# Kernel optimization log

Hardware: AMD Instinct MI355X
Metric: run time of the kernel (lower is better)

Reference implementation:

```python
import jax, jax.numpy as jnp
import numpy as np

B, P, N = 32, 64, 8192
EPS_CASE = 0.0001  # hard-coded threshold in fc_of_edge's tf.where


def setup_inputs() -> dict:
    key = jax.random.key(0)
    k1, k2 = jax.random.split(key)
    points = jax.random.normal(k1, (B, P, 2), dtype=jnp.float32)
    # phi grid comes from fc_tensor[0, 0, :] in the original ctor; use angles in [0, 2*pi)
    phi = jax.random.uniform(k2, (N,), dtype=jnp.float32) * (2.0 * np.pi)
    return {"points": points, "phi": phi}


def reference(points, phi):
    # q(phi) = [cos(phi), sin(phi) - 1], shape [2, N]
    q = jnp.stack([jnp.cos(phi), jnp.sin(phi) - 1.0])
    cross = jnp.array([[0.0, -1.0], [1.0, 0.0]], dtype=points.dtype)
    q_cross = cross @ q                                   # [2, N]
    scale = 1.0 / jnp.abs(q[0] ** 2 + q[1] ** 2)          # [N], real

    # vectorize the python edge loop: edge k is (points[:, k-1], points[:, k])
    p1 = points                                           # [B, P, 2]
    p0 = jnp.roll(points, 1, axis=1)                      # [B, P, 2]
    d = p1 - p0

    dot = lambda a, b: jnp.einsum('bpi,in->bpn', a, b)    # [B, P, N]
    dp0q = dot(p0, q)
    dp1q = dot(p1, q)
    ddq = dot(d, q)
    ddqc = dot(d, q_cross)

    j = jnp.complex64(1j)
    f_p0 = -jnp.exp(j * dp0q)                             # c = 0 in fc_of_phi
    f_p1 = -jnp.exp(j * dp1q)

    mask = jnp.abs(ddq) >= EPS_CASE
    ddq_safe = jnp.where(mask, ddq, 1.0)                  # avoid div-by-~0 in unused branch
    case1 = scale * ddqc * (f_p1 - f_p0) / ddq_safe
    case2 = scale * ddqc * (-j) * jnp.exp(j * dp0q)
    res = jnp.where(mask, case1, case2)                   # [B, P, N] complex64

    sum_res = jnp.sum(res, axis=1)                        # [B, N]
    # original: concat(real, imag) along axis=1 of [B, 1, N] -> [B, 2, N]
    return jnp.stack([jnp.real(sum_res), jnp.imag(sum_res)], axis=1)
```

## Files before the change

### kernel.cpp

```cpp
#include <hip/hip_runtime.h>
#include <math.h>

#define BATCH 32
#define PTS   64
#define NPHI  8192

__device__ __forceinline__ void fast_sincosf(float xf, float* s, float* c) {
    const double PIO2_HI = 1.57079632679489661923e+00;
    const double PIO2_LO = 6.12323399573676603587e-17;

    const float kf = __builtin_rintf(__fmul_rn(xf, 0.63661977236758138243f));
    const int   qi = (int)kf;
    const double kd = (double)qi;
    const double x  = (double)xf;

    double r = __builtin_fma(-kd, PIO2_HI, x);
    r = __builtin_fma(-kd, PIO2_LO, r);
    const double r2 = r * r;

    double ps = 1.58969099521155010221e-10;
    ps = __builtin_fma(ps, r2, -2.50507602534068634195e-08);
    ps = __builtin_fma(ps, r2,  2.75573137070700676789e-06);
    ps = __builtin_fma(ps, r2, -1.98412698298579493134e-04);
    ps = __builtin_fma(ps, r2,  8.33333333332248946124e-03);
    ps = __builtin_fma(ps, r2, -1.66666666666666324348e-01);
    const double sinr = __builtin_fma(r * r2, ps, r);

    double pc = -1.13596475577881948265e-11;
    pc = __builtin_fma(pc, r2,  2.08757232129817482790e-09);
    pc = __builtin_fma(pc, r2, -2.75573143513906633035e-07);
    pc = __builtin_fma(pc, r2,  2.48015872894767294178e-05);
    pc = __builtin_fma(pc, r2, -1.38888888888741095749e-03);
    pc = __builtin_fma(pc, r2,  4.16666666666666019037e-02);
    const double cosr = __builtin_fma(r2 * r2, pc, __builtin_fma(-0.5, r2, 1.0));

    const float sf = (float)sinr, cf = (float)cosr;
    const bool sw = (qi & 1);
    const float ss = sw ? cf : sf;
    const float cc = sw ? sf : cf;
    *s = (qi & 2)       ? -ss : ss;
    *c = ((qi + 1) & 2) ? -cc : cc;
}

__global__ __launch_bounds__(256, 8) void scatter_polygon_kernel(
    const float* __restrict__ points,
    const float* __restrict__ phi,
    float* __restrict__ out)
{
    __shared__ float spts[2 * PTS];

    const int b = blockIdx.y;
    const int tid = threadIdx.x;
    const int h = tid & 1;
    const int n = blockIdx.x * 128 + (tid >> 1);

    if (tid < 2 * PTS) {
        spts[tid] = points[b * 2 * PTS + tid];
    }
    __syncthreads();

    const float ph = phi[n];
    float sph, cph;
    fast_sincosf(ph, &sph, &cph);
    const float q0  = cph;
    const float q1  = __fsub_rn(sph, 1.0f);
    const float nq1 = -q1;
    const float scale =
        1.0f / fabsf(__fadd_rn(__fmul_rn(q0, q0), __fmul_rn(q1, q1)));

    const int p0i = h ? (PTS / 2 - 1) : (PTS - 1);
    float xp = spts[2 * p0i];
    float yp = spts[2 * p0i + 1];
    const float dp_prev = __fadd_rn(__fmul_rn(xp, q0), __fmul_rn(yp, q1));
    float s0, c0;
    fast_sincosf(dp_prev, &s0, &c0);

    float accR = 0.0f, accI = 0.0f;
    const int pbase = h * (PTS / 2);

    #pragma unroll 4
    for (int i = 0; i < PTS / 2; ++i) {
        const int p = pbase + i;
        const float x = spts[2 * p];
        const float y = spts[2 * p + 1];
        const float dp_cur = __fadd_rn(__fmul_rn(x, q0), __fmul_rn(y, q1));
        float s1, c1;
        fast_sincosf(dp_cur, &s1, &c1);

        const float dx = __fsub_rn(x, xp);
        const float dy = __fsub_rn(y, yp);
        const float ddq  = __fadd_rn(__fmul_rn(dx, q0),  __fmul_rn(dy, q1));
        const float ddqc = __fadd_rn(__fmul_rn(dx, nq1), __fmul_rn(dy, q0));
        const float t = __fmul_rn(scale, ddqc);

        const float dR = __fsub_rn(c0, c1);
        const float dI = __fsub_rn(s0, s1);
        const bool  m1 = (fabsf(ddq) >= 1e-4f);
        const float inv = __builtin_amdgcn_rcpf(m1 ? ddq : 1.0f);
        const float ti = t * inv;
        const float r1R = ti * dR;
        const float r1I = ti * dI;
        const float r2R = t * s0;
        const float r2I = -t * c0;

        accR += m1 ? r1R : r2R;
        accI += m1 ? r1I : r2I;

        xp = x; yp = y; c0 = c1; s0 = s1;
    }

    const float totR = accR + __shfl_xor(accR, 1);
    const float totI = accI + __shfl_xor(accI, 1);

    if (h == 0) {
        out[(size_t)b * 2 * NPHI + n]        = totR;
        out[(size_t)b * 2 * NPHI + NPHI + n] = totI;
    }
}

extern "C" void kernel_launch(void* const* d_in, const int* in_sizes, int n_in,
                              void* d_out, int out_size, void* d_ws, size_t ws_size,
                              hipStream_t stream) {
    const float* points = (const float*)d_in[0];
    const float* phi    = (const float*)d_in[1];
    float* out          = (float*)d_out;

    dim3 grid(NPHI / 128, BATCH);
    scatter_polygon_kernel<<<grid, 256, 0, stream>>>(points, phi, out);
}
```

Measured before the change: 80.16 us.

## Use float32 sincos in inner loop and hoist scale out of accumulation

```diff
diff --git a/kernel.cpp b/kernel.cpp
--- a/kernel.cpp
+++ b/kernel.cpp
@@ -5,29 +5,27 @@
 #define PTS   64
 #define NPHI  8192
 
-__device__ __forceinline__ void fast_sincosf(float xf, float* s, float* c) {
+__device__ __forceinline__ void sincosf_f64(float xf, float* s, float* c) {
     const double PIO2_HI = 1.57079632679489661923e+00;
     const double PIO2_LO = 6.12323399573676603587e-17;
 
     const float kf = __builtin_rintf(__fmul_rn(xf, 0.63661977236758138243f));
     const int   qi = (int)kf;
-    const double kd = (double)qi;
+    const double kd = (double)kf;
     const double x  = (double)xf;
 
     double r = __builtin_fma(-kd, PIO2_HI, x);
     r = __builtin_fma(-kd, PIO2_LO, r);
     const double r2 = r * r;
 
-    double ps = 1.58969099521155010221e-10;
-    ps = __builtin_fma(ps, r2, -2.50507602534068634195e-08);
+    double ps = -2.50507602534068634195e-08;
     ps = __builtin_fma(ps, r2,  2.75573137070700676789e-06);
     ps = __builtin_fma(ps, r2, -1.98412698298579493134e-04);
     ps = __builtin_fma(ps, r2,  8.33333333332248946124e-03);
     ps = __builtin_fma(ps, r2, -1.66666666666666324348e-01);
     const double sinr = __builtin_fma(r * r2, ps, r);
 
-    double pc = -1.13596475577881948265e-11;
-    pc = __builtin_fma(pc, r2,  2.08757232129817482790e-09);
+    double pc =  2.08757232129817482790e-09;
     pc = __builtin_fma(pc, r2, -2.75573143513906633035e-07);
     pc = __builtin_fma(pc, r2,  2.48015872894767294178e-05);
     pc = __builtin_fma(pc, r2, -1.38888888888741095749e-03);
@@ -38,6 +36,34 @@
     const bool sw = (qi & 1);
     const float ss = sw ? cf : sf;
     const float cc = sw ? sf : cf;
+    *s = (qi & 2)       ? -ss : ss;
+    *c = ((qi + 1) & 2) ? -cc : cc;
+}
+
+__device__ __forceinline__ void sincosf_f32(float x, float* s, float* c) {
+    const float C1 = 1.5707969665527344f;
+    const float C2 = -6.3975783777e-7f;
+
+    const float kf = __builtin_rintf(x * 0.63661977236758f);
+    const int   qi = (int)kf;
+    const float r1 = __builtin_fmaf(-kf, C1, x);
+    const float r  = __builtin_fmaf(-kf, C2, r1);
+    const float r2 = r * r;
+
+    float ps = __builtin_fmaf(2.75573137e-06f, r2, -1.98412698e-04f);
+    ps = __builtin_fmaf(ps, r2,  8.33333333e-03f);
+    ps = __builtin_fmaf(ps, r2, -1.66666667e-01f);
+    const float sr = __builtin_fmaf(r * r2, ps, r);
+
+    float pc = __builtin_fmaf(-2.75573144e-07f, r2, 2.48015873e-05f);
+    pc = __builtin_fmaf(pc, r2, -1.38888889e-03f);
+    pc = __builtin_fmaf(pc, r2,  4.16666667e-02f);
+    const float u  = __builtin_fmaf(r2 * r2, pc, -(0.5f * r2));
+    const float cr = 1.0f + u;
+
+    const bool sw = (qi & 1);
+    const float ss = sw ? cr : sr;
+    const float cc = sw ? sr : cr;
     *s = (qi & 2)       ? -ss : ss;
     *c = ((qi + 1) & 2) ? -cc : cc;
 }
@@ -61,7 +87,7 @@
 
     const float ph = phi[n];
     float sph, cph;
-    fast_sincosf(ph, &sph, &cph);
+    sincosf_f64(ph, &sph, &cph);
     const float q0  = cph;
     const float q1  = __fsub_rn(sph, 1.0f);
     const float nq1 = -q1;
@@ -73,7 +99,7 @@
     float yp = spts[2 * p0i + 1];
     const float dp_prev = __fadd_rn(__fmul_rn(xp, q0), __fmul_rn(yp, q1));
     float s0, c0;
-    fast_sincosf(dp_prev, &s0, &c0);
+    sincosf_f32(dp_prev, &s0, &c0);
 
     float accR = 0.0f, accI = 0.0f;
     const int pbase = h * (PTS / 2);
@@ -85,32 +111,27 @@
         const float y = spts[2 * p + 1];
         const float dp_cur = __fadd_rn(__fmul_rn(x, q0), __fmul_rn(y, q1));
         float s1, c1;
-        fast_sincosf(dp_cur, &s1, &c1);
+        sincosf_f32(dp_cur, &s1, &c1);
 
         const float dx = __fsub_rn(x, xp);
         const float dy = __fsub_rn(y, yp);
         const float ddq  = __fadd_rn(__fmul_rn(dx, q0),  __fmul_rn(dy, q1));
         const float ddqc = __fadd_rn(__fmul_rn(dx, nq1), __fmul_rn(dy, q0));
-        const float t = __fmul_rn(scale, ddqc);
 
+        const bool  m1  = (fabsf(ddq) >= 1e-4f);
+        const float inv = __builtin_amdgcn_rcpf(ddq);
         const float dR = __fsub_rn(c0, c1);
         const float dI = __fsub_rn(s0, s1);
-        const bool  m1 = (fabsf(ddq) >= 1e-4f);
-        const float inv = __builtin_amdgcn_rcpf(m1 ? ddq : 1.0f);
-        const float ti = t * inv;
-        const float r1R = ti * dR;
-        const float r1I = ti * dI;
-        const float r2R = t * s0;
-        const float r2I = -t * c0;
-
-        accR += m1 ? r1R : r2R;
-        accI += m1 ? r1I : r2I;
+        const float gR = m1 ? (dR * inv) : s0;
+        const float gI = m1 ? (dI * inv) : (-c0);
+        accR = __builtin_fmaf(ddqc, gR, accR);
+        accI = __builtin_fmaf(ddqc, gI, accI);
 
         xp = x; yp = y; c0 = c1; s0 = s1;
     }
 
-    const float totR = accR + __shfl_xor(accR, 1);
-    const float totI = accI + __shfl_xor(accI, 1);
+    const float totR = scale * (accR + __shfl_xor(accR, 1));
+    const float totI = scale * (accI + __shfl_xor(accI, 1));
 
     if (h == 0) {
         out[(size_t)b * 2 * NPHI + n]        = totR;
```

New measurement: 74.79 us. 1.07x faster.
